# Optimization experiments

Hardware: AMD Instinct MI355X
Metric: run time of the kernel (lower is better)

Reference implementation:

```python
import jax, jax.numpy as jnp
import numpy as np

SIGMA = 1.0
CONST = 0.5 * np.log(2.0 * np.pi * SIGMA ** 2)  # scalar constant from __init__


def setup_inputs() -> dict:
    key = jax.random.key(0)
    k1, k2 = jax.random.split(key)
    predicted_points = jax.random.normal(k1, (4, 4096, 3), dtype=jnp.float32)
    gt_means = jax.random.normal(k2, (4, 4096, 3), dtype=jnp.float32)
    return {"predicted_points": predicted_points, "gt_means": gt_means}


def reference(predicted_points, gt_means):
    # pairwise squared distances: (B, N, M)
    diff = predicted_points[:, :, None, :] - gt_means[:, None, :, :]  # (B,N,M,D)
    sq_distances = jnp.sum(diff * diff, axis=-1)
    log_probs = -CONST - sq_distances / (2.0 * SIGMA ** 2)
    # stable logsumexp over mixture components M
    log_likelihood = jax.nn.logsumexp(log_probs, axis=2)  # (B, N)
    loss = -jnp.mean(log_likelihood)
    return loss
```

## Files before the change

kernel.cpp:

```cpp
#include <hip/hip_runtime.h>
#include <math.h>

#define BATCH 4
#define NPTS 4096
#define NMIX 4096
#define THREADS 256
#define PPB 16
#define PPT 8
#define SCH 128
#define MSTAGE 2048
#define PASSES (NMIX / MSTAGE)
#define MPT (MSTAGE / SCH)
#define NBLOCKS ((BATCH * NPTS) / PPB)

#define LN2 0.6931471805599453f
#define CONST_TERM 0.9189385332046727f
#define INV_COUNT (1.0f / (float)(BATCH * NPTS))
#define SEXP_K    12102203.0f
#define SEXP_BIAS 1.06488094e9f

typedef float v2f __attribute__((ext_vector_type(2)));

__device__ __forceinline__ float fast_log2(float x) {
#if __has_builtin(__builtin_amdgcn_logf)
  return __builtin_amdgcn_logf(x);
#else
  return log2f(x);
#endif
}

__global__ __launch_bounds__(THREADS) void gm_main(
    const float* __restrict__ pred, const float* __restrict__ gt,
    float* __restrict__ bsum) {
  __shared__ float4 gsh[MSTAGE];
  __shared__ float wpart[64];
  float* comb = (float*)gsh;

  const int t = threadIdx.x;
  const int b = blockIdx.x >> 8;
  const int n0 = (blockIdx.x & 255) * PPB;
  const int c = t >> 1;
  const int pi = (t & 1) * PPT;

  v2f px[4], py[4], pz[4];
  float accx[4], accy[4];
#pragma unroll
  for (int k = 0; k < 4; ++k) {
    const float* p = pred + ((size_t)(b * NPTS + n0 + pi + 2 * k)) * 3;
    px[k] = (v2f){p[0], p[3]};
    py[k] = (v2f){p[1], p[4]};
    pz[k] = (v2f){p[2], p[5]};
    accx[k] = 0.f;
    accy[k] = 0.f;
  }

  for (int q = 0; q < PASSES; ++q) {
    __syncthreads();
#pragma unroll
    for (int k2 = 0; k2 < MSTAGE / THREADS; ++k2) {
      int s = t + k2 * THREADS;
      const float* g = gt + ((size_t)(b * NMIX + q * MSTAGE + s)) * 3;
      float gx = g[0], gy = g[1], gz = g[2];
      float n2 = fmaf(gx, gx, fmaf(gy, gy, gz * gz));
      gsh[s] = make_float4(SEXP_K * gx, SEXP_K * gy, SEXP_K * gz,
                           fmaf(n2, -0.5f * SEXP_K, SEXP_BIAS));
    }
    __syncthreads();

    const float4* gbase = gsh + c;
#pragma unroll 4
    for (int j = 0; j < MPT; ++j) {
      float4 gv = gbase[SCH * j];
      v2f bx = {gv.x, gv.x}, by = {gv.y, gv.y};
      v2f bz = {gv.z, gv.z}, bw = {gv.w, gv.w};
#pragma unroll
      for (int k = 0; k < 4; ++k) {
        v2f d = __builtin_elementwise_fma(px[k], bx,
                __builtin_elementwise_fma(py[k], by,
                __builtin_elementwise_fma(pz[k], bz, bw)));
        accx[k] += __builtin_bit_cast(float, (int)d.x);
        accy[k] += __builtin_bit_cast(float, (int)d.y);
      }
    }
  }

  __syncthreads();

#pragma unroll
  for (int k = 0; k < 4; ++k) {
    comb[c * (PPB + 1) + pi + 2 * k]     = accx[k];
    comb[c * (PPB + 1) + pi + 2 * k + 1] = accy[k];
  }
  __syncthreads();

  {
    const int p = t & 15, g = t >> 4;
    float s = 0.f;
#pragma unroll
    for (int j = 0; j < 8; ++j) s += comb[(g * 8 + j) * (PPB + 1) + p];
    s += __shfl_down(s, 32, 64);
    s += __shfl_down(s, 16, 64);
    if ((t & 63) < 16) wpart[(t >> 6) * 16 + (t & 15)] = s;
  }
  __syncthreads();

  if (t < 16) {
    float s = wpart[t] + wpart[16 + t] + wpart[32 + t] + wpart[48 + t];
    const float* p = pred + ((size_t)(b * NPTS + n0 + t)) * 3;
    float hp2 = 0.5f * (p[0] * p[0] + p[1] * p[1] + p[2] * p[2]);
    float ll = (LN2 * fast_log2(s) - hp2) * INV_COUNT;
#pragma unroll
    for (int off = 8; off > 0; off >>= 1) ll += __shfl_down(ll, off, 16);
    if (t == 0) bsum[blockIdx.x] = ll;
  }
}

__global__ __launch_bounds__(THREADS) void gm_reduce(
    const float* __restrict__ bsum, float* __restrict__ out) {
  const int t = threadIdx.x;
  float v = (bsum[t] + bsum[t + 256]) + (bsum[t + 512] + bsum[t + 768]);
  for (int off = 32; off > 0; off >>= 1) v += __shfl_down(v, off, 64);
  __shared__ float w[4];
  if ((t & 63) == 0) w[t >> 6] = v;
  __syncthreads();
  if (t == 0) out[0] = CONST_TERM - ((w[0] + w[1]) + (w[2] + w[3]));
}

extern "C" void kernel_launch(void* const* d_in, const int* in_sizes, int n_in,
                              void* d_out, int out_size, void* d_ws, size_t ws_size,
                              hipStream_t stream) {
  const float* pred = (const float*)d_in[0];
  const float* gt   = (const float*)d_in[1];
  float* out = (float*)d_out;
  float* bsum = (float*)d_ws;

  gm_main<<<NBLOCKS, THREADS, 0, stream>>>(pred, gt, bsum);
  gm_reduce<<<1, THREADS, 0, stream>>>(bsum, out);
}
```

Before: 17.16 us.

## Precompute mixture table in a prep kernel and read it directly from global memory

Adds a separate gm_prep kernel that turns gt_means into scaled float4 entries once, so each main block no longer recomputes and stages 2048-entry chunks into LDS. The main kernel drops shared staging and __syncthreads and reads the table straight from global memory (L2/L1 resident, 256 KB). The accumulators also become packed v2f adds. This cuts the 32 KB LDS footprint and the per-block redundant preprocessing, which should raise occupancy. The cost is an extra kernel launch and reliance on cache bandwidth for the inner-loop loads.

Result: slower. 21.32 us (+24.2%).

```diff
diff --git a/kernel.cpp b/kernel.cpp
--- a/kernel.cpp
+++ b/kernel.cpp
@@ -8,9 +8,7 @@
 #define PPB 16
 #define PPT 8
 #define SCH 128
-#define MSTAGE 2048
-#define PASSES (NMIX / MSTAGE)
-#define MPT (MSTAGE / SCH)
+#define JITER (NMIX / SCH)
 #define NBLOCKS ((BATCH * NPTS) / PPB)
 
 #define LN2 0.6931471805599453f
@@ -29,12 +27,21 @@
 #endif
 }
 
+__global__ __launch_bounds__(THREADS) void gm_prep(
+    const float* __restrict__ gt, float4* __restrict__ tab) {
+  const int i = blockIdx.x * THREADS + threadIdx.x;
+  const float* g = gt + (size_t)i * 3;
+  float gx = g[0], gy = g[1], gz = g[2];
+  float n2 = fmaf(gx, gx, fmaf(gy, gy, gz * gz));
+  tab[i] = make_float4(SEXP_K * gx, SEXP_K * gy, SEXP_K * gz,
+                       fmaf(n2, -0.5f * SEXP_K, SEXP_BIAS));
+}
+
 __global__ __launch_bounds__(THREADS) void gm_main(
-    const float* __restrict__ pred, const float* __restrict__ gt,
+    const float4* __restrict__ tab, const float* __restrict__ pred,
     float* __restrict__ bsum) {
-  __shared__ float4 gsh[MSTAGE];
+  __shared__ float comb[SCH * (PPB + 1)];
   __shared__ float wpart[64];
-  float* comb = (float*)gsh;
 
   const int t = threadIdx.x;
   const int b = blockIdx.x >> 8;
@@ -42,54 +49,38 @@
   const int c = t >> 1;
   const int pi = (t & 1) * PPT;
 
-  v2f px[4], py[4], pz[4];
-  float accx[4], accy[4];
+  v2f px[4], py[4], pz[4], acc[4];
 #pragma unroll
   for (int k = 0; k < 4; ++k) {
     const float* p = pred + ((size_t)(b * NPTS + n0 + pi + 2 * k)) * 3;
     px[k] = (v2f){p[0], p[3]};
     py[k] = (v2f){p[1], p[4]};
     pz[k] = (v2f){p[2], p[5]};
-    accx[k] = 0.f;
-    accy[k] = 0.f;
+    acc[k] = (v2f){0.f, 0.f};
   }
 
-  for (int q = 0; q < PASSES; ++q) {
-    __syncthreads();
+  const float4* tb = tab + (size_t)b * NMIX + c;
+#pragma unroll 8
+  for (int j = 0; j < JITER; ++j) {
+    float4 gv = tb[(size_t)SCH * j];
+    v2f bx = {gv.x, gv.x}, by = {gv.y, gv.y};
+    v2f bz = {gv.z, gv.z}, bw = {gv.w, gv.w};
 #pragma unroll
-    for (int k2 = 0; k2 < MSTAGE / THREADS; ++k2) {
-      int s = t + k2 * THREADS;
-      const float* g = gt + ((size_t)(b * NMIX + q * MSTAGE + s)) * 3;
-      float gx = g[0], gy = g[1], gz = g[2];
-      float n2 = fmaf(gx, gx, fmaf(gy, gy, gz * gz));
-      gsh[s] = make_float4(SEXP_K * gx, SEXP_K * gy, SEXP_K * gz,
-                           fmaf(n2, -0.5f * SEXP_K, SEXP_BIAS));
-    }
-    __syncthreads();
-
-    const float4* gbase = gsh + c;
-#pragma unroll 4
-    for (int j = 0; j < MPT; ++j) {
-      float4 gv = gbase[SCH * j];
-      v2f bx = {gv.x, gv.x}, by = {gv.y, gv.y};
-      v2f bz = {gv.z, gv.z}, bw = {gv.w, gv.w};
-#pragma unroll
-      for (int k = 0; k < 4; ++k) {
-        v2f d = __builtin_elementwise_fma(px[k], bx,
-                __builtin_elementwise_fma(py[k], by,
-                __builtin_elementwise_fma(pz[k], bz, bw)));
-        accx[k] += __builtin_bit_cast(float, (int)d.x);
-        accy[k] += __builtin_bit_cast(float, (int)d.y);
-      }
+    for (int k = 0; k < 4; ++k) {
+      v2f d = __builtin_elementwise_fma(px[k], bx,
+              __builtin_elementwise_fma(py[k], by,
+              __builtin_elementwise_fma(pz[k], bz, bw)));
+      v2f e;
+      e.x = __builtin_bit_cast(float, (int)d.x);
+      e.y = __builtin_bit_cast(float, (int)d.y);
+      acc[k] += e;
     }
   }
 
-  __syncthreads();
-
 #pragma unroll
   for (int k = 0; k < 4; ++k) {
-    comb[c * (PPB + 1) + pi + 2 * k]     = accx[k];
-    comb[c * (PPB + 1) + pi + 2 * k + 1] = accy[k];
+    comb[c * (PPB + 1) + pi + 2 * k]     = acc[k].x;
+    comb[c * (PPB + 1) + pi + 2 * k + 1] = acc[k].y;
   }
   __syncthreads();
 
@@ -132,8 +123,11 @@
   const float* pred = (const float*)d_in[0];
   const float* gt   = (const float*)d_in[1];
   float* out = (float*)d_out;
-  float* bsum = (float*)d_ws;
 
-  gm_main<<<NBLOCKS, THREADS, 0, stream>>>(pred, gt, bsum);
+  float4* tab = (float4*)d_ws;
+  float* bsum = (float*)d_ws + 4 * BATCH * NMIX;
+
+  gm_prep<<<(BATCH * NMIX) / THREADS, THREADS, 0, stream>>>(gt, tab);
+  gm_main<<<NBLOCKS, THREADS, 0, stream>>>(tab, pred, bsum);
   gm_reduce<<<1, THREADS, 0, stream>>>(bsum, out);
 }
```

## Pack mixture components in pairs and remap threads to 4 points x pairs

Applied to the files above, without the earlier changes.

Changes the shared-memory layout so each pair of mixture components is stored interleaved (x0,x1,y0,y1,z0,z1,w0,w1), and remaps threads so each handles 4 points against pairs of components. Packed FMAs now vectorise across components instead of points, with inline v_pk_fma_f32 asm. Point coordinates are broadcast into both lanes. Global loads of gt use float2 reads. The aim is fewer LDS reads per FMA and better packed-math utilisation. The tradeoff is two float4 LDS loads per iteration and more complex staging.

Measured after the change: 17.17 us. About the same (+0.1%).

```diff
diff --git a/kernel.cpp b/kernel.cpp
--- a/kernel.cpp
+++ b/kernel.cpp
@@ -6,11 +6,9 @@
 #define NMIX 4096
 #define THREADS 256
 #define PPB 16
-#define PPT 8
-#define SCH 128
 #define MSTAGE 2048
 #define PASSES (NMIX / MSTAGE)
-#define MPT (MSTAGE / SCH)
+#define JITER 16
 #define NBLOCKS ((BATCH * NPTS) / PPB)
 
 #define LN2 0.6931471805599453f
@@ -29,6 +27,12 @@
 #endif
 }
 
+__device__ __forceinline__ v2f pk_fma(v2f a, v2f b, v2f c) {
+  v2f d;
+  asm("v_pk_fma_f32 %0, %1, %2, %3" : "=v"(d) : "v"(a), "v"(b), "v"(c));
+  return d;
+}
+
 __global__ __launch_bounds__(THREADS) void gm_main(
     const float* __restrict__ pred, const float* __restrict__ gt,
     float* __restrict__ bsum) {
@@ -39,47 +43,51 @@
   const int t = threadIdx.x;
   const int b = blockIdx.x >> 8;
   const int n0 = (blockIdx.x & 255) * PPB;
-  const int c = t >> 1;
-  const int pi = (t & 1) * PPT;
+  const int pl = t & 3;
+  const int ml = t >> 2;
 
-  v2f px[4], py[4], pz[4];
-  float accx[4], accy[4];
+  v2f px2[4], py2[4], pz2[4], acc[4];
 #pragma unroll
   for (int k = 0; k < 4; ++k) {
-    const float* p = pred + ((size_t)(b * NPTS + n0 + pi + 2 * k)) * 3;
-    px[k] = (v2f){p[0], p[3]};
-    py[k] = (v2f){p[1], p[4]};
-    pz[k] = (v2f){p[2], p[5]};
-    accx[k] = 0.f;
-    accy[k] = 0.f;
+    const float* p = pred + ((size_t)(b * NPTS + n0 + pl * 4 + k)) * 3;
+    px2[k] = (v2f){p[0], p[0]};
+    py2[k] = (v2f){p[1], p[1]};
+    pz2[k] = (v2f){p[2], p[2]};
+    acc[k] = (v2f){0.f, 0.f};
   }
 
   for (int q = 0; q < PASSES; ++q) {
     __syncthreads();
 #pragma unroll
-    for (int k2 = 0; k2 < MSTAGE / THREADS; ++k2) {
-      int s = t + k2 * THREADS;
-      const float* g = gt + ((size_t)(b * NMIX + q * MSTAGE + s)) * 3;
-      float gx = g[0], gy = g[1], gz = g[2];
-      float n2 = fmaf(gx, gx, fmaf(gy, gy, gz * gz));
-      gsh[s] = make_float4(SEXP_K * gx, SEXP_K * gy, SEXP_K * gz,
-                           fmaf(n2, -0.5f * SEXP_K, SEXP_BIAS));
+    for (int i = 0; i < 4; ++i) {
+      int s = t + i * THREADS;
+      const float2* g = (const float2*)(gt +
+          ((size_t)(b * NMIX + q * MSTAGE + 2 * s)) * 3);
+      float2 g01 = g[0], g23 = g[1], g45 = g[2];
+      float n20 = fmaf(g01.x, g01.x, fmaf(g01.y, g01.y, g23.x * g23.x));
+      float n21 = fmaf(g23.y, g23.y, fmaf(g45.x, g45.x, g45.y * g45.y));
+      gsh[2 * s]     = make_float4(SEXP_K * g01.x, SEXP_K * g23.y,
+                                   SEXP_K * g01.y, SEXP_K * g45.x);
+      gsh[2 * s + 1] = make_float4(SEXP_K * g23.x, SEXP_K * g45.y,
+                                   fmaf(n20, -0.5f * SEXP_K, SEXP_BIAS),
+                                   fmaf(n21, -0.5f * SEXP_K, SEXP_BIAS));
     }
     __syncthreads();
 
-    const float4* gbase = gsh + c;
 #pragma unroll 4
-    for (int j = 0; j < MPT; ++j) {
-      float4 gv = gbase[SCH * j];
-      v2f bx = {gv.x, gv.x}, by = {gv.y, gv.y};
-      v2f bz = {gv.z, gv.z}, bw = {gv.w, gv.w};
+    for (int j = 0; j < JITER; ++j) {
+      int s = ml + 64 * j;
+      float4 a = gsh[2 * s];
+      float4 c4 = gsh[2 * s + 1];
+      v2f gx2 = (v2f){a.x, a.y}, gy2 = (v2f){a.z, a.w};
+      v2f gz2 = (v2f){c4.x, c4.y}, w2 = (v2f){c4.z, c4.w};
 #pragma unroll
       for (int k = 0; k < 4; ++k) {
-        v2f d = __builtin_elementwise_fma(px[k], bx,
-                __builtin_elementwise_fma(py[k], by,
-                __builtin_elementwise_fma(pz[k], bz, bw)));
-        accx[k] += __builtin_bit_cast(float, (int)d.x);
-        accy[k] += __builtin_bit_cast(float, (int)d.y);
+        v2f d = pk_fma(pz2[k], gz2, w2);
+        d = pk_fma(py2[k], gy2, d);
+        d = pk_fma(px2[k], gx2, d);
+        acc[k].x += __builtin_bit_cast(float, (int)d.x);
+        acc[k].y += __builtin_bit_cast(float, (int)d.y);
       }
     }
   }
@@ -87,20 +95,18 @@
   __syncthreads();
 
 #pragma unroll
-  for (int k = 0; k < 4; ++k) {
-    comb[c * (PPB + 1) + pi + 2 * k]     = accx[k];
-    comb[c * (PPB + 1) + pi + 2 * k + 1] = accy[k];
-  }
+  for (int k = 0; k < 4; ++k)
+    comb[ml * (PPB + 1) + pl * 4 + k] = acc[k].x + acc[k].y;
   __syncthreads();
 
   {
-    const int p = t & 15, g = t >> 4;
+    const int col = t & 15, grp = t >> 4;
     float s = 0.f;
 #pragma unroll
-    for (int j = 0; j < 8; ++j) s += comb[(g * 8 + j) * (PPB + 1) + p];
+    for (int r = 0; r < 4; ++r) s += comb[(grp * 4 + r) * (PPB + 1) + col];
     s += __shfl_down(s, 32, 64);
     s += __shfl_down(s, 16, 64);
-    if ((t & 63) < 16) wpart[(t >> 6) * 16 + (t & 15)] = s;
+    if ((t & 63) < 16) wpart[(t >> 6) * 16 + col] = s;
   }
   __syncthreads();
 
```
